# Kernel tuning notes

Hardware: AMD Instinct MI355X
Metric: run time of the kernel (lower is better)

Reference implementation:

```python
import jax, jax.numpy as jnp
import numpy as np

LMAX = 4
NC = (LMAX + 1) ** 2          # 25 spherical coefficients
L0 = LMAX + 1                 # number of m=0 coefficients
SPHERE = 128
CIN1 = 2 * SPHERE             # concat(source, target) channels
HID = 64
HEADS = 8
ALPHA_C = 64
VAL_C = 16
OUT_C = 128
GRID = 2 * (LMAX + 1)         # S2 grid resolution
N_NODES = 2500
N_EDGES = 25000
MAX_ELEM = 90
EDGE_IN = 128 + 2 * 64        # distance basis + src/tgt atom embeddings
M_SIZES = [LMAX - m + 1 for m in range(1, LMAX + 1)]  # l-count per |m|>0
RAD_OUT = L0 * CIN1 + sum(s * CIN1 for s in M_SIZES)  # 3840

def _lm(l, m):
    return l * l + l + m
_p = [_lm(l, 0) for l in range(LMAX + 1)]
for m in range(1, LMAX + 1):
    _p += [_lm(l, -m) for l in range(m, LMAX + 1)]
    _p += [_lm(l, m) for l in range(m, LMAX + 1)]
PERM = np.asarray(_p)             # l-primary -> m-primary
INV_PERM = np.argsort(PERM)       # m-primary -> l-primary
EXPAND = np.concatenate([np.full(2 * l + 1, l) for l in range(LMAX + 1)])

def _layernorm(x, g, b, eps=1e-5):
    mu = jnp.mean(x, axis=-1, keepdims=True)
    var = jnp.mean((x - mu) ** 2, axis=-1, keepdims=True)
    return (x - mu) * jax.lax.rsqrt(var + eps) * g + b

def _so2_conv(xm, fc0_w, fc0_b, wms, cin, mout, extra, rad):
    # xm: [E, NC, cin] in m-primary layout. Per-order SO(2) 'complex' conv.
    E = xm.shape[0]
    x0 = xm[:, :L0].reshape(E, L0 * cin)
    off_rad = L0 * cin
    if rad is not None:
        x0 = x0 * rad[:, :off_rad]
    x0 = x0 @ fc0_w + fc0_b
    x0_extra = None
    if extra:
        x0_extra = x0[:, :extra]
        x0 = x0[:, extra:]
    outs = [x0.reshape(E, L0, mout)]
    off = L0
    for i, sz in enumerate(M_SIZES):
        xb = xm[:, off:off + 2 * sz].reshape(E, 2, sz * cin)
        if rad is not None:
            xb = xb * rad[:, off_rad:off_rad + sz * cin][:, None, :]
            off_rad += sz * cin
        y = xb @ wms[i]                         # [E, 2, 2*mout*sz]
        half = y.shape[-1] // 2
        yr, yi = y[..., :half], y[..., half:]
        o = jnp.stack([yr[:, 0] - yi[:, 1], yr[:, 1] + yi[:, 0]], axis=1)
        outs.append(o.reshape(E, 2 * sz, mout))
        off += 2 * sz
    return jnp.concatenate(outs, axis=1), x0_extra

def _segment_softmax(logits, seg, num_segments):
    mx = jax.ops.segment_max(logits, seg, num_segments=num_segments)
    ex = jnp.exp(logits - mx[seg])
    s = jax.ops.segment_sum(ex, seg, num_segments=num_segments)
    return ex / (s[seg] + 1e-16)

def setup_inputs():
    key = jax.random.key(0)
    ks = iter(jax.random.split(key, 64))
    def nrm(shape, scale=1.0):
        return jax.random.normal(next(ks), shape, dtype=jnp.float32) * scale
    def lin(i, o):
        return nrm((i, o), i ** -0.5)
    inp = {}
    inp['x'] = nrm((N_NODES, NC, SPHERE))
    inp['edge_distance'] = nrm((N_EDGES, 128))
    inp['src_table'] = jax.random.uniform(next(ks), (MAX_ELEM, 64), jnp.float32, -0.001, 0.001)
    inp['tgt_table'] = jax.random.uniform(next(ks), (MAX_ELEM, 64), jnp.float32, -0.001, 0.001)
    inp['rad_w1'] = lin(EDGE_IN, 64); inp['rad_b1'] = jnp.zeros((64,), jnp.float32)
    inp['rad_ln1_g'] = jnp.ones((64,), jnp.float32); inp['rad_ln1_b'] = jnp.zeros((64,), jnp.float32)
    inp['rad_w2'] = lin(64, 64); inp['rad_b2'] = jnp.zeros((64,), jnp.float32)
    inp['rad_ln2_g'] = jnp.ones((64,), jnp.float32); inp['rad_ln2_b'] = jnp.zeros((64,), jnp.float32)
    inp['rad_w3'] = lin(64, RAD_OUT); inp['rad_b3'] = jnp.zeros((RAD_OUT,), jnp.float32)
    inp['wigner'] = nrm((N_EDGES, NC, NC), NC ** -0.5)
    extra1 = HEADS * ALPHA_C + HID
    inp['c1_fc0_w'] = lin(L0 * CIN1, L0 * HID + extra1)
    inp['c1_fc0_b'] = jnp.zeros((L0 * HID + extra1,), jnp.float32)
    for i, sz in enumerate(M_SIZES):
        inp['c1_wm%d' % (i + 1)] = lin(sz * CIN1, 2 * HID * sz)
    inp['to_grid'] = nrm((GRID, GRID, NC), NC ** -0.5)
    inp['from_grid'] = nrm((GRID, GRID, NC), float(GRID * GRID) ** -0.5)
    inp['alpha_ln_g'] = jnp.ones((ALPHA_C,), jnp.float32)
    inp['alpha_ln_b'] = jnp.zeros((ALPHA_C,), jnp.float32)
    std = ALPHA_C ** -0.5
    inp['alpha_dot'] = jax.random.uniform(next(ks), (HEADS, ALPHA_C), jnp.float32, -std, std)
    vout = HEADS * VAL_C
    inp['c2_fc0_w'] = lin(L0 * HID, L0 * vout)
    inp['c2_fc0_b'] = jnp.zeros((L0 * vout,), jnp.float32)
    for i, sz in enumerate(M_SIZES):
        inp['c2_wm%d' % (i + 1)] = lin(sz * HID, 2 * vout * sz)
    inp['proj_w'] = nrm((L0, OUT_C, vout), vout ** -0.5)
    inp['proj_b'] = jnp.zeros((OUT_C,), jnp.float32)
    inp['atomic_numbers'] = jax.random.randint(next(ks), (N_NODES,), 0, MAX_ELEM)
    inp['edge_index'] = jax.random.randint(next(ks), (2, N_EDGES), 0, N_NODES)
    return inp

def reference(x, edge_distance, src_table, tgt_table,
              rad_w1, rad_b1, rad_ln1_g, rad_ln1_b, rad_w2, rad_b2, rad_ln2_g, rad_ln2_b, rad_w3, rad_b3,
              wigner, c1_fc0_w, c1_fc0_b, c1_wm1, c1_wm2, c1_wm3, c1_wm4,
              to_grid, from_grid, alpha_ln_g, alpha_ln_b, alpha_dot,
              c2_fc0_w, c2_fc0_b, c2_wm1, c2_wm2, c2_wm3, c2_wm4, proj_w, proj_b,
              atomic_numbers, edge_index):
    E = edge_index.shape[1]
    N = x.shape[0]
    src, tgt = edge_index[0], edge_index[1]
    # invariant edge scalars: distance basis + source/target atom embeddings
    x_edge = jnp.concatenate([edge_distance, src_table[atomic_numbers[src]], tgt_table[atomic_numbers[tgt]]], axis=1)
    # gather node embeddings to edges, rotate into edge frame (Wigner-D)
    msg = jnp.concatenate([x[src], x[tgt]], axis=2)          # [E, NC, 2*SPHERE]
    msg = jnp.einsum('eml,elc->emc', wigner, msg)
    msg = msg[:, PERM]                                        # m-primary layout
    # radial MLP producing per-(m,l,channel) edge weights
    h = jax.nn.silu(_layernorm(x_edge @ rad_w1 + rad_b1, rad_ln1_g, rad_ln1_b))
    h = jax.nn.silu(_layernorm(h @ rad_w2 + rad_b2, rad_ln2_g, rad_ln2_b))
    rad = h @ rad_w3 + rad_b3                                 # [E, RAD_OUT]
    extra1 = HEADS * ALPHA_C + HID
    msg, x0_extra = _so2_conv(msg, c1_fc0_w, c1_fc0_b, (c1_wm1, c1_wm2, c1_wm3, c1_wm4), CIN1, HID, extra1, rad)
    x0_alpha = x0_extra[:, :HEADS * ALPHA_C]
    x0_gate = x0_extra[:, HEADS * ALPHA_C:]
    # separable S2 activation: scalar SiLU on l=0, grid SiLU on l>0
    msg_l = msg[:, INV_PERM]
    grid = jax.nn.silu(jnp.einsum('bai,eic->ebac', to_grid, msg_l))
    s2 = jnp.einsum('bai,ebac->eic', from_grid, grid)
    msg_l = jnp.concatenate([jax.nn.silu(x0_gate)[:, None, :], s2[:, 1:]], axis=1)
    # second SO(2) conv (internal weights, no radial)
    msg_m = msg_l[:, PERM]
    msg_m, _ = _so2_conv(msg_m, c2_fc0_w, c2_fc0_b, (c2_wm1, c2_wm2, c2_wm3, c2_wm4), HID, HEADS * VAL_C, None, None)
    msg_l = msg_m[:, INV_PERM]
    # attention logits (LayerNorm + SmoothLeakyReLU(0.2) + dot)
    a = _layernorm(x0_alpha.reshape(E, HEADS, ALPHA_C), alpha_ln_g, alpha_ln_b)
    a = 0.6 * a + 0.4 * a * (2.0 * jax.nn.sigmoid(a) - 1.0)
    logits = jnp.einsum('ehk,hk->eh', a, alpha_dot)
    # rotate messages back to global frame (wigner_inv = wigner^T)
    msg_l = jnp.einsum('eml,emc->elc', wigner, msg_l)
    alpha = _segment_softmax(logits, tgt, N)                  # [E, HEADS]
    v = msg_l.reshape(E, NC, HEADS, VAL_C) * alpha[:, None, :, None]
    node = jax.ops.segment_sum(v.reshape(E, NC, HEADS * VAL_C), tgt, num_segments=N)
    # SO3_LinearV2 projection: per-degree linear, bias only on l=0
    out = jnp.einsum('nmi,moi->nmo', node, proj_w[EXPAND])
    out = out.at[:, 0, :].add(proj_b)
    return out
```

## Files before the change

kernel.cpp:

```cpp
#include <hip/hip_runtime.h>
#include <cstddef>

typedef unsigned short u16;
typedef __attribute__((ext_vector_type(8))) short short8;
typedef __attribute__((ext_vector_type(4))) float float4v;

__constant__ int c_PERM[25] = {0,2,6,12,20, 1,5,11,19, 3,7,13,21, 4,10,18, 8,14,22, 9,17, 15,23, 16,24};
__constant__ int c_ROFF[25] = {0,256,512,768,1024, 1280,1536,1792,2048, 1280,1536,1792,2048,
                               2304,2560,2816, 2304,2560,2816, 3072,3328, 3072,3328, 3584,3584};
__constant__ int c_EXPAND[25] = {0,1,1,1,2,2,2,2,2,3,3,3,3,3,3,3,4,4,4,4,4,4,4,4,4};

static constexpr int PERM_CE[25] = {0,2,6,12,20, 1,5,11,19, 3,7,13,21, 4,10,18, 8,14,22, 9,17, 15,23, 16,24};
static constexpr int INV_CE[25]  = {0,5,1,9,13, 6,2,10,16,19, 14,7,3,11,17, 21,23,20,15,8, 4,12,18,22,24};

__device__ __forceinline__ float wsum64(float v){
#pragma unroll
  for(int m=32;m>0;m>>=1) v += __shfl_xor(v, m, 64);
  return v;
}
__device__ __forceinline__ float siluf(float x){ return x/(1.f+expf(-x)); }

__device__ __forceinline__ void bsplit(float v, u16 &h, u16 &l){
  unsigned u = __float_as_uint(v);
  unsigned hb = (u + 0x7FFFu + ((u>>16)&1u)) >> 16;
  h = (u16)hb;
  float r = v - __uint_as_float(hb<<16);
  unsigned u2 = __float_as_uint(r);
  l = (u16)((u2 + 0x7FFFu + ((u2>>16)&1u)) >> 16);
}

__global__ __launch_bounds__(256) void wtrans_kernel(const float* __restrict__ W, u16* __restrict__ Wh, u16* __restrict__ Wl, int K, int C2){
  int idx = blockIdx.x*256 + threadIdx.x;
  int K2 = 2*K;
  if(idx >= C2*K2) return;
  int n = idx / K2, k2 = idx % K2;
  int half = C2>>1;
  float v;
  if(k2 < K) v = W[k2*C2 + n];
  else { int k = k2-K; v = (n<half) ? -W[k*C2 + half + n] : W[k*C2 + n - half]; }
  u16 h,l; bsplit(v,h,l);
  Wh[idx]=h; Wl[idx]=l;
}

__global__ __launch_bounds__(256) void fctrans_kernel(const float* __restrict__ W, u16* __restrict__ Wh, u16* __restrict__ Wl, int K, int N){
  int idx = blockIdx.x*256 + threadIdx.x;
  if(idx >= N*K) return;
  int n = idx / K, k = idx % K;
  u16 h,l; bsplit(W[(size_t)k*N + n],h,l);
  Wh[idx]=h; Wl[idx]=l;
}

__global__ __launch_bounds__(256) void ptrans_kernel(const float* __restrict__ pw, float* __restrict__ pwt){
  int idx = blockIdx.x*256+threadIdx.x;
  if(idx >= 5*16384) return;
  int l = idx>>14, r = idx & 16383, i = r>>7, o = r&127;
  pwt[idx] = pw[(l<<14) + (o<<7) + i];
}

__global__ __launch_bounds__(256) void hist_kernel(const int* __restrict__ tgt_all, int* __restrict__ cnt, int E){
  int idx = blockIdx.x*256+threadIdx.x;
  if(idx>=E) return;
  atomicAdd(&cnt[tgt_all[idx]], 1);
}
__global__ __launch_bounds__(256) void scan_kernel(const int* __restrict__ cnt, int* __restrict__ basearr, int* __restrict__ cur, int NN){
  __shared__ int sh[256];
  __shared__ int carry;
  if(threadIdx.x==0) carry = 0;
  __syncthreads();
  for(int t0=0; t0<NN; t0+=256){
    int i = t0 + threadIdx.x;
    int v = (i<NN)? cnt[i] : 0;
    sh[threadIdx.x]=v; __syncthreads();
    for(int off=1; off<256; off<<=1){
      int add = (threadIdx.x>=off)? sh[threadIdx.x-off]:0; __syncthreads();
      sh[threadIdx.x]+=add; __syncthreads();
    }
    int excl = carry + sh[threadIdx.x]-v;
    if(i<NN){ basearr[i]=excl; cur[i]=excl; }
    __syncthreads();
    if(threadIdx.x==255) carry += sh[255];
    __syncthreads();
  }
}
__global__ __launch_bounds__(256) void scatter_kernel(const int* __restrict__ ei, int* __restrict__ cur,
    int* __restrict__ order, int* __restrict__ srcs, int* __restrict__ tgts, int E){
  int idx = blockIdx.x*256+threadIdx.x;
  if(idx>=E) return;
  int t = ei[E+idx];
  int pos = atomicAdd(&cur[t], 1);
  order[pos] = idx;
  tgts[pos] = t;
  srcs[pos] = ei[idx];
}

__global__ __launch_bounds__(64) void radial_kernel(
    const float* __restrict__ ed, const float* __restrict__ st, const float* __restrict__ tt,
    const float* __restrict__ w1, const float* __restrict__ b1, const float* __restrict__ g1, const float* __restrict__ bb1,
    const float* __restrict__ w2, const float* __restrict__ b2, const float* __restrict__ g2, const float* __restrict__ bb2,
    const int* __restrict__ an, const int* __restrict__ order,
    const int* __restrict__ src, const int* __restrict__ tgt,
    u16* __restrict__ h2h, u16* __restrict__ h2l){
  int e = blockIdx.x; int lane = threadIdx.x;
  __shared__ float xe[256];
  __shared__ float h1s[64];
  int eo = order[e];
  int s = src[e], t = tgt[e];
  xe[lane]      = ed[(size_t)eo*128 + lane];
  xe[64+lane]   = ed[(size_t)eo*128 + 64 + lane];
  int as = an[s], at = an[t];
  xe[128+lane]  = st[as*64 + lane];
  xe[192+lane]  = tt[at*64 + lane];
  __syncthreads();
  float acc = b1[lane];
  for(int k=0;k<256;k++) acc += xe[k]*w1[k*64+lane];
  float mu = wsum64(acc)*(1.f/64.f);
  float d = acc - mu;
  float var = wsum64(d*d)*(1.f/64.f);
  float nrm = d*rsqrtf(var+1e-5f)*g1[lane]+bb1[lane];
  h1s[lane] = siluf(nrm);
  __syncthreads();
  float acc2 = b2[lane];
  for(int k=0;k<64;k++) acc2 += h1s[k]*w2[k*64+lane];
  mu = wsum64(acc2)*(1.f/64.f);
  d = acc2-mu;
  var = wsum64(d*d)*(1.f/64.f);
  nrm = d*rsqrtf(var+1e-5f)*g2[lane]+bb2[lane];
  u16 h,l; bsplit(siluf(nrm),h,l);
  h2h[(size_t)e*64+lane]=h; h2l[(size_t)e*64+lane]=l;
}

struct GrpArgs {
  const u16* Ah[6]; const u16* Al[6];
  const u16* Bh[6]; const u16* Bl[6];
  const float* bias[6]; float* C1[6]; float* C2[6];
  int lda[6]; int K[6]; int ldc1[6]; int ldc2[6]; int split[6];
  int xoff[7]; int ng; int M; int gx; int gy;
};

__global__ __launch_bounds__(256) void mgemm_kernel(GrpArgs a){
  __shared__ __align__(16) u16 Ash[2][4096];
  __shared__ __align__(16) u16 Asl[2][4096];
  __shared__ __align__(16) u16 Bsh[2][4096];
  __shared__ __align__(16) u16 Bsl[2][4096];

  int b = blockIdx.x;
  int xcd = b & 7, i = b >> 3;
  int pbase = a.gx >> 3, prem = a.gx & 7;
  int s = pbase + (xcd < prem ? 1 : 0);
  if(i >= s * a.gy) return;
  int o = xcd*pbase + (xcd < prem ? xcd : prem);
  int xt = o + (i % s);
  int yt = i / s;

  int g = 0;
  while(g+1 < a.ng && xt >= a.xoff[g+1]) g++;
  int n0 = (xt - a.xoff[g])*128, m0 = yt*128;
  const int M = a.M, K = a.K[g], lda = a.lda[g];
  const u16* __restrict__ Ah = a.Ah[g]; const u16* __restrict__ Al = a.Al[g];
  const u16* __restrict__ Bh = a.Bh[g]; const u16* __restrict__ Bl = a.Bl[g];
  int t = threadIdx.x;
  int r0 = t>>2, kblk = t&3, k80 = kblk*8;
  int ar0 = m0 + r0; if(ar0 >= M) ar0 = M-1;
  int ar1 = m0 + r0 + 64; if(ar1 >= M) ar1 = M-1;
  const u16* Ap0h = Ah + (size_t)ar0*lda + k80;
  const u16* Ap1h = Ah + (size_t)ar1*lda + k80;
  const u16* Ap0l = Al + (size_t)ar0*lda + k80;
  const u16* Ap1l = Al + (size_t)ar1*lda + k80;
  const u16* Bp0h = Bh + (size_t)(n0+r0)*K + k80;
  const u16* Bp1h = Bh + (size_t)(n0+r0+64)*K + k80;
  const u16* Bp0l = Bl + (size_t)(n0+r0)*K + k80;
  const u16* Bp1l = Bl + (size_t)(n0+r0+64)*K + k80;
  int pcbS = kblk ^ ((r0>>1)&3);
  int sA = r0*32 + pcbS*8;
  int sB = sA + 64*32;

  int wave = t>>6, lane = t&63;
  int wr = wave>>1, wc = wave&1;
  int ml = lane&15, q = lane>>4;
  int pcbA = q ^ ((ml>>1)&3);
  int aoff = (wr*64 + ml)*32 + pcbA*8;
  int boff = (wc*64 + ml)*32 + pcbA*8;

  float4v acc[4][4];
#pragma unroll
  for(int i2=0;i2<4;i2++)
#pragma unroll
    for(int j=0;j<4;j++) acc[i2][j] = 0.f;

  short8 cva[4], cvb[4];
  cva[0] = *(const short8*)(Ap0h); cva[1] = *(const short8*)(Ap1h);
  cva[2] = *(const short8*)(Ap0l); cva[3] = *(const short8*)(Ap1l);
  cvb[0] = *(const short8*)(Bp0h); cvb[1] = *(const short8*)(Bp1h);
  cvb[2] = *(const short8*)(Bp0l); cvb[3] = *(const short8*)(Bp1l);

  int p = 0;
  for(int k0=0; k0<K; k0+=32){
    *(short8*)(&Ash[p][sA]) = cva[0];
    *(short8*)(&Ash[p][sB]) = cva[1];
    *(short8*)(&Asl[p][sA]) = cva[2];
    *(short8*)(&Asl[p][sB]) = cva[3];
    *(short8*)(&Bsh[p][sA]) = cvb[0];
    *(short8*)(&Bsh[p][sB]) = cvb[1];
    *(short8*)(&Bsl[p][sA]) = cvb[2];
    *(short8*)(&Bsl[p][sB]) = cvb[3];
    __syncthreads();
    if(k0+32 < K){
      int kn = k0+32;
      cva[0] = *(const short8*)(Ap0h + kn); cva[1] = *(const short8*)(Ap1h + kn);
      cva[2] = *(const short8*)(Ap0l + kn); cva[3] = *(const short8*)(Ap1l + kn);
      cvb[0] = *(const short8*)(Bp0h + kn); cvb[1] = *(const short8*)(Bp1h + kn);
      cvb[2] = *(const short8*)(Bp0l + kn); cvb[3] = *(const short8*)(Bp1l + kn);
    }
    short8 afh[4], afl[4];
#pragma unroll
    for(int i2=0;i2<4;i2++){
      afh[i2] = *(const short8*)(&Ash[p][aoff + i2*512]);
      afl[i2] = *(const short8*)(&Asl[p][aoff + i2*512]);
    }
#pragma unroll
    for(int j=0;j<4;j++){
      short8 bfh = *(const short8*)(&Bsh[p][boff + j*512]);
      short8 bfl = *(const short8*)(&Bsl[p][boff + j*512]);
#pragma unroll
      for(int i2=0;i2<4;i2++){
        acc[i2][j] = __builtin_amdgcn_mfma_f32_16x16x32_bf16(afh[i2], bfh, acc[i2][j], 0,0,0);
        acc[i2][j] = __builtin_amdgcn_mfma_f32_16x16x32_bf16(afh[i2], bfl, acc[i2][j], 0,0,0);
        acc[i2][j] = __builtin_amdgcn_mfma_f32_16x16x32_bf16(afl[i2], bfh, acc[i2][j], 0,0,0);
      }
    }
    p ^= 1;
  }
  const float* bias = a.bias[g];
  int split = a.split[g];
  float* C1 = a.C1[g]; float* C2 = a.C2[g];
  int ldc1 = a.ldc1[g], ldc2 = a.ldc2[g];
#pragma unroll
  for(int i2=0;i2<4;i2++){
    int rowb = m0 + wr*64 + i2*16 + q*4;
#pragma unroll
    for(int r=0;r<4;r++){
      int row = rowb + r;
      if(row < M){
#pragma unroll
        for(int j=0;j<4;j++){
          int col = n0 + wc*64 + j*16 + ml;
          float v = acc[i2][j][r];
          if(bias) v += bias[col];
          if(col < split) C1[(size_t)row*ldc1 + col] = v;
          else            C2[(size_t)row*ldc2 + (col-split)] = v;
        }
      }
    }
  }
}

__global__ __launch_bounds__(256) void wigner1_kernel(
    const float* __restrict__ x, const float* __restrict__ wigner_all,
    const int* __restrict__ order, const int* __restrict__ src, const int* __restrict__ tgt,
    const float* __restrict__ rad, u16* __restrict__ msg1h, u16* __restrict__ msg1l){
  int e = blockIdx.x; int t = threadIdx.x;
  __shared__ float wig[625];
  __shared__ float4 cat4[1600];
  int eo = order[e];
  int s = src[e], tg = tgt[e];
  for(int i=t;i<625;i+=256) wig[i] = wigner_all[(size_t)eo*625 + i];
  const float4* xs = (const float4*)(x + (size_t)s*3200);
  const float4* xt = (const float4*)(x + (size_t)tg*3200);
  for(int idx=t; idx<1600; idx+=256){
    int l = idx>>6, slot = idx&63;
    cat4[idx] = (slot<32) ? xs[l*32 + slot] : xt[l*32 + (slot-32)];
  }
  __syncthreads();
  int wave = t>>6, lane = t&63;
  for(int p=wave; p<25; p+=4){
    int pl = c_PERM[p];
    float4 acc = {0.f,0.f,0.f,0.f};
#pragma unroll
    for(int l=0;l<25;l++){
      float w = wig[pl*25 + l];
      float4 c = cat4[l*64 + lane];
      acc.x += w*c.x; acc.y += w*c.y; acc.z += w*c.z; acc.w += w*c.w;
    }
    float4 rd = *(const float4*)(rad + (size_t)e*3840 + c_ROFF[p] + lane*4);
    acc.x*=rd.x; acc.y*=rd.y; acc.z*=rd.z; acc.w*=rd.w;
    u16 h0,h1,h2,h3,l0,l1,l2,l3;
    bsplit(acc.x,h0,l0); bsplit(acc.y,h1,l1); bsplit(acc.z,h2,l2); bsplit(acc.w,h3,l3);
    size_t base = (size_t)e*6400 + p*256 + lane*4;
    *(uint2*)(msg1h + base) = make_uint2((unsigned)h0 | ((unsigned)h1<<16), (unsigned)h2 | ((unsigned)h3<<16));
    *(uint2*)(msg1l + base) = make_uint2((unsigned)l0 | ((unsigned)l1<<16), (unsigned)l2 | ((unsigned)l3<<16));
  }
}

__global__ __launch_bounds__(64) void grid_kernel(
    const float* __restrict__ msg2, const float* __restrict__ x0e,
    const float* __restrict__ tg, const float* __restrict__ fg,
    u16* __restrict__ m2h, u16* __restrict__ m2l){
  int e = blockIdx.x; int lane = threadIdx.x;
  float r[25];
#pragma unroll
  for(int i=0;i<25;i++) r[i] = msg2[((size_t)e*25 + INV_CE[i])*64 + lane];
  float s2[25];
#pragma unroll
  for(int i=0;i<25;i++) s2[i]=0.f;
  for(int g=0; g<100; g++){
    float tv=0.f;
#pragma unroll
    for(int i=0;i<25;i++) tv += tg[g*25+i]*r[i];
    tv = siluf(tv);
#pragma unroll
    for(int i=0;i<25;i++) s2[i] += fg[g*25+i]*tv;
  }
  float gate = siluf(x0e[(size_t)e*576 + 512 + lane]);
#pragma unroll
  for(int p=0;p<25;p++){
    int lp = PERM_CE[p];
    float v = (lp==0) ? gate : s2[lp];
    u16 h,l; bsplit(v,h,l);
    size_t idx = ((size_t)e*25+p)*64 + lane;
    m2h[idx]=h; m2l[idx]=l;
  }
}

__global__ __launch_bounds__(64) void alpha_kernel(
    const float* __restrict__ x0e, const float* __restrict__ g, const float* __restrict__ b,
    const float* __restrict__ adot, const int* __restrict__ tgt,
    float* __restrict__ exb, float* __restrict__ ssum){
  int e = blockIdx.x; int lane = threadIdx.x;
  int t = tgt[e];
  float gg = g[lane], bb = b[lane];
  for(int h=0;h<8;h++){
    float v = x0e[(size_t)e*576 + h*64 + lane];
    float mu = wsum64(v)*(1.f/64.f);
    float d = v-mu;
    float var = wsum64(d*d)*(1.f/64.f);
    float a = d*rsqrtf(var+1e-5f)*gg+bb;
    float sig = 1.f/(1.f+expf(-a));
    float a2 = 0.6f*a + 0.4f*a*(2.f*sig-1.f);
    float p = a2*adot[h*64+lane];
    float lg = wsum64(p);
    if(lane==0){
      float ex = expf(lg);
      exb[e*8+h]=ex;
      atomicAdd(&ssum[t*8+h], ex);
    }
  }
}

__global__ __launch_bounds__(256) void agg_kernel(
    const float* __restrict__ wigner_all, const float* __restrict__ msg3,
    const float* __restrict__ exb, const int* __restrict__ order,
    const int* __restrict__ basearr, const int* __restrict__ cnt,
    float* __restrict__ node, int e0, int e1){
  int n = blockIdx.x; int t = threadIdx.x;
  int b0 = basearr[n], c = cnt[n];
  int lo = b0 > e0 ? b0 : e0;
  int hi = (b0+c) < e1 ? (b0+c) : e1;
  if(lo >= hi) return;
  int lg = t>>5;
  int c4 = t&31;
  __shared__ float wig2[625];
  __shared__ float m3s[3200];
  float4v acc[4];
#pragma unroll
  for(int k=0;k<4;k++) acc[k] = 0.f;
  float* nb = node + (size_t)n*3200;
#pragma unroll
  for(int k=0;k<4;k++){ int l = lg + 8*k; if(l<25) acc[k] = *(const float4v*)(nb + l*128 + c4*4); }
  for(int j=lo;j<hi;j++){
    int e = order[j];
    int el = j - e0;
    __syncthreads();
    for(int i=t;i<625;i+=256){ int q=i/25, l=i%25; wig2[i] = wigner_all[((size_t)e*25 + c_PERM[q])*25 + l]; }
    for(int i=t;i<800;i+=256) ((float4*)m3s)[i] = ((const float4*)(msg3 + (size_t)el*3200))[i];
    __syncthreads();
    float ex = exb[el*8 + (c4>>2)];
    float4v tmp[4];
#pragma unroll
    for(int k=0;k<4;k++) tmp[k] = 0.f;
    for(int q=0;q<25;q++){
      float4v m = *(const float4v*)(m3s + q*128 + c4*4);
#pragma unroll
      for(int k=0;k<4;k++){
        int l = lg + 8*k;
        float w = (l<25) ? wig2[q*25 + l] : 0.f;
        tmp[k] += w*m;
      }
    }
#pragma unroll
    for(int k=0;k<4;k++) acc[k] += ex*tmp[k];
  }
#pragma unroll
  for(int k=0;k<4;k++){ int l = lg + 8*k; if(l<25) *(float4v*)(nb + l*128 + c4*4) = acc[k]; }
}

__global__ __launch_bounds__(256) void proj_kernel(
    const float* __restrict__ node, const float* __restrict__ ssum,
    const float* __restrict__ pwt, const float* __restrict__ proj_b,
    float* __restrict__ out, int NN){
  int n0 = blockIdx.x*2; int t = threadIdx.x;
  __shared__ float nd[2][3200];
  __shared__ float inv[2][8];
  if(t<16){
    int j=t>>3, h=t&7;
    int n=n0+j; if(n>=NN) n=NN-1;
    inv[j][h] = 1.f/(ssum[n*8+h] + 1e-16f);
  }
  __syncthreads();
  int n1 = (n0+1 < NN) ? (n0+1) : (NN-1);
  for(int i=t;i<3200;i+=256){
    int h = (i&127)>>4;
    nd[0][i] = node[(size_t)n0*3200 + i] * inv[0][h];
    nd[1][i] = node[(size_t)n1*3200 + i] * inv[1][h];
  }
  __syncthreads();
  int o = t&127, half = t>>7;
  for(int p=half;p<25;p+=2){
    int l = c_EXPAND[p];
    const float* w = pwt + l*16384;
    float a0=0.f, a1=0.f;
    for(int i=0;i<128;i++){
      float wv = w[i*128+o];
      a0 += nd[0][p*128+i]*wv;
      a1 += nd[1][p*128+i]*wv;
    }
    float bs = (p==0)? proj_b[o] : 0.f;
    out[((size_t)n0*25+p)*128 + o] = a0 + bs;
    if(n0+1 < NN) out[((size_t)(n0+1)*25+p)*128 + o] = a1 + bs;
  }
}

extern "C" void kernel_launch(void* const* d_in, const int* in_sizes, int n_in,
                              void* d_out, int out_size, void* d_ws, size_t ws_size,
                              hipStream_t stream) {
  const float* x           = (const float*)d_in[0];
  const float* edge_dist   = (const float*)d_in[1];
  const float* src_table   = (const float*)d_in[2];
  const float* tgt_table   = (const float*)d_in[3];
  const float* rad_w1      = (const float*)d_in[4];
  const float* rad_b1      = (const float*)d_in[5];
  const float* rad_ln1_g   = (const float*)d_in[6];
  const float* rad_ln1_b   = (const float*)d_in[7];
  const float* rad_w2      = (const float*)d_in[8];
  const float* rad_b2      = (const float*)d_in[9];
  const float* rad_ln2_g   = (const float*)d_in[10];
  const float* rad_ln2_b   = (const float*)d_in[11];
  const float* rad_w3      = (const float*)d_in[12];
  const float* rad_b3      = (const float*)d_in[13];
  const float* wigner      = (const float*)d_in[14];
  const float* c1_fc0_w    = (const float*)d_in[15];
  const float* c1_fc0_b    = (const float*)d_in[16];
  const float* c1_wm[4]    = {(const float*)d_in[17],(const float*)d_in[18],(const float*)d_in[19],(const float*)d_in[20]};
  const float* to_grid     = (const float*)d_in[21];
  const float* from_grid   = (const float*)d_in[22];
  const float* alpha_ln_g  = (const float*)d_in[23];
  const float* alpha_ln_b  = (const float*)d_in[24];
  const float* alpha_dot   = (const float*)d_in[25];
  const float* c2_fc0_w    = (const float*)d_in[26];
  const float* c2_fc0_b    = (const float*)d_in[27];
  const float* c2_wm[4]    = {(const float*)d_in[28],(const float*)d_in[29],(const float*)d_in[30],(const float*)d_in[31]};
  const float* proj_w      = (const float*)d_in[32];
  const float* proj_b      = (const float*)d_in[33];
  const int*   atomic_nums = (const int*)d_in[34];
  const int*   edge_index  = (const int*)d_in[35];
  float* out = (float*)d_out;
  (void)n_in; (void)out_size;

  const int E  = in_sizes[35]/2;
  const int NN = in_sizes[34];

  const int K1[4] = {1024, 768, 512, 256}, C1c[4] = {512, 384, 256, 128};
  const int K2[4] = {256, 192, 128, 64},  C2c[4] = {1024, 768, 512, 256};
  const size_t W3T = 3840*64;
  const size_t FC1 = 896*1280;
  const size_t W1S[4] = {512*2048, 384*1536, 256*1024, 128*512};
  const size_t FC2 = 640*320;
  const size_t W2S[4] = {1024*512, 768*384, 512*256, 256*128};
  const size_t WSUM = W3T + FC1 + W1S[0]+W1S[1]+W1S[2]+W1S[3] + FC2 + W2S[0]+W2S[1]+W2S[2]+W2S[3];
  const size_t persist = (size_t)NN*8 + (size_t)NN*3200 + WSUM
                       + 81920 + (size_t)3*NN + (size_t)3*E + 8192;
  const size_t wfl = ws_size / sizeof(float);
  const int copts[10] = {25000, 12500, 6250, 5000, 3125, 2500, 1250, 625, 250, 125};
  int C = 125;
  for(int i=0;i<10;i++){
    size_t hc = (size_t)(copts[i]+1)/2;
    size_t need = (size_t)copts[i]*(6400+576+8) + hc*3840 + persist;
    if(need <= wfl){ C = copts[i]; break; }
  }
  const int nch = (E + C - 1)/C;
  const size_t halfC = (size_t)(C+1)/2;

  float* ws = (float*)d_ws;
  u16* msg1h = (u16*)ws;
  u16* msg1l = msg1h + (size_t)C*6400;
  u16* m2h   = (u16*)ws;
  u16* m2l   = m2h + (size_t)C*1600;
  float* msg3 = ws + (size_t)C*1600;
  float* rad  = ws + (size_t)C*6400;
  float* msg2 = rad;
  float* x0e  = rad + halfC*3840;
  u16* h2h = (u16*)x0e;
  u16* h2l = h2h + halfC*64;
  float* exb  = x0e + (size_t)C*576;
  float* ssum = exb + (size_t)C*8;
  float* node = ssum + (size_t)NN*8;
  u16* wb = (u16*)(node + (size_t)NN*3200);
  u16 *w3h = wb, *w3l = w3h + W3T;
  u16 *f1h = w3l + W3T, *f1l = f1h + FC1;
  u16 *w1h[4], *w1l[4];
  u16* p = f1l + FC1;
  for(int i=0;i<4;i++){ w1h[i]=p; w1l[i]=p+W1S[i]; p += 2*W1S[i]; }
  u16 *f2h = p, *f2l = f2h + FC2; p = f2l + FC2;
  u16 *w2h[4], *w2l[4];
  for(int i=0;i<4;i++){ w2h[i]=p; w2l[i]=p+W2S[i]; p += 2*W2S[i]; }
  float* pwt = (float*)p;
  int* cntb  = (int*)(pwt + 81920);
  int* baseb = cntb + NN;
  int* curb  = baseb + NN;
  int* order = curb + NN;
  int* srcs  = order + E;
  int* tgts  = srcs + E;

  hipMemsetAsync(node, 0, (size_t)NN*3200*sizeof(float), stream);
  hipMemsetAsync(ssum, 0, (size_t)NN*8*sizeof(float), stream);
  hipMemsetAsync(cntb, 0, (size_t)NN*sizeof(int), stream);

  hist_kernel<<<(E+255)/256, 256, 0, stream>>>(edge_index + E, cntb, E);
  scan_kernel<<<1, 256, 0, stream>>>(cntb, baseb, curb, NN);
  scatter_kernel<<<(E+255)/256, 256, 0, stream>>>(edge_index, curb, order, srcs, tgts, E);

  fctrans_kernel<<<((int)W3T+255)/256, 256, 0, stream>>>(rad_w3, w3h, w3l, 64, 3840);
  fctrans_kernel<<<((int)FC1+255)/256, 256, 0, stream>>>(c1_fc0_w, f1h, f1l, 1280, 896);
  fctrans_kernel<<<((int)FC2+255)/256, 256, 0, stream>>>(c2_fc0_w, f2h, f2l, 320, 640);
  for(int i=0;i<4;i++)
    wtrans_kernel<<<((int)W1S[i]*2+255)/256, 256, 0, stream>>>(c1_wm[i], w1h[i], w1l[i], K1[i], C1c[i]);
  for(int i=0;i<4;i++)
    wtrans_kernel<<<((int)W2S[i]*2+255)/256, 256, 0, stream>>>(c2_wm[i], w2h[i], w2l[i], K2[i], C2c[i]);
  ptrans_kernel<<<320, 256, 0, stream>>>(proj_w, pwt);

  auto launchM = [&](GrpArgs &ga, int gx, int gy){
    ga.gx = gx; ga.gy = gy;
    int base = gx>>3, rem = gx&7;
    int maxs = base + (rem?1:0);
    mgemm_kernel<<<8*maxs*gy, 256, 0, stream>>>(ga);
  };

  const int OFF1[4] = {5,13,19,23};
  for(int ch=0; ch<nch; ch++){
    int e0 = ch*C;
    int ce = (E - e0 < C) ? (E - e0) : C;
    int mt = (ce+127)/128;

    int half1 = (ce+1)/2;
    for(int hh=0; hh<2; hh++){
      int h0 = hh ? half1 : 0;
      int he = hh ? (ce - half1) : half1;
      if(he <= 0) continue;
      radial_kernel<<<he, 64, 0, stream>>>(edge_dist, src_table, tgt_table,
          rad_w1, rad_b1, rad_ln1_g, rad_ln1_b, rad_w2, rad_b2, rad_ln2_g, rad_ln2_b,
          atomic_nums, order + e0 + h0, srcs + e0 + h0, tgts + e0 + h0, h2h, h2l);
      {
        GrpArgs ga = {};
        ga.ng = 1; ga.M = he;
        ga.Ah[0]=h2h; ga.Al[0]=h2l; ga.Bh[0]=w3h; ga.Bl[0]=w3l;
        ga.bias[0]=rad_b3; ga.C1[0]=rad; ga.C2[0]=nullptr;
        ga.lda[0]=64; ga.K[0]=64; ga.ldc1[0]=3840; ga.ldc2[0]=0; ga.split[0]=3840;
        ga.xoff[0]=0; ga.xoff[1]=30;
        launchM(ga, 30, (he+127)/128);
      }
      wigner1_kernel<<<he, 256, 0, stream>>>(x, wigner, order + e0 + h0, srcs + e0 + h0, tgts + e0 + h0,
          rad, msg1h + (size_t)h0*6400, msg1l + (size_t)h0*6400);
    }

    {
      GrpArgs ga = {};
      ga.ng = 5; ga.M = ce;
      ga.Ah[0]=msg1h; ga.Al[0]=msg1l; ga.Bh[0]=f1h; ga.Bl[0]=f1l;
      ga.bias[0]=c1_fc0_b; ga.C1[0]=x0e; ga.C2[0]=msg2;
      ga.lda[0]=6400; ga.K[0]=1280; ga.ldc1[0]=576; ga.ldc2[0]=1600; ga.split[0]=576;
      int xo = 7;
      ga.xoff[0]=0; ga.xoff[1]=7;
      for(int i=0;i<4;i++){
        int gidx = i+1;
        ga.Ah[gidx]=msg1h + (size_t)OFF1[i]*256; ga.Al[gidx]=msg1l + (size_t)OFF1[i]*256;
        ga.Bh[gidx]=w1h[i]; ga.Bl[gidx]=w1l[i];
        ga.bias[gidx]=nullptr; ga.C1[gidx]=msg2 + OFF1[i]*64; ga.C2[gidx]=nullptr;
        ga.lda[gidx]=6400; ga.K[gidx]=2*K1[i]; ga.ldc1[gidx]=1600; ga.ldc2[gidx]=0; ga.split[gidx]=C1c[i];
        xo += C1c[i]/128;
        ga.xoff[gidx+1]=xo;
      }
      launchM(ga, xo, mt);
    }

    grid_kernel<<<ce, 64, 0, stream>>>(msg2, x0e, to_grid, from_grid, m2h, m2l);
    alpha_kernel<<<ce, 64, 0, stream>>>(x0e, alpha_ln_g, alpha_ln_b, alpha_dot, tgts + e0, exb, ssum);

    {
      GrpArgs ga = {};
      ga.ng = 5; ga.M = ce;
      ga.Ah[0]=m2h; ga.Al[0]=m2l; ga.Bh[0]=f2h; ga.Bl[0]=f2l;
      ga.bias[0]=c2_fc0_b; ga.C1[0]=msg3; ga.C2[0]=nullptr;
      ga.lda[0]=1600; ga.K[0]=320; ga.ldc1[0]=3200; ga.ldc2[0]=0; ga.split[0]=640;
      int xo = 5;
      ga.xoff[0]=0; ga.xoff[1]=5;
      for(int i=0;i<4;i++){
        int gidx = i+1;
        ga.Ah[gidx]=m2h + (size_t)OFF1[i]*64; ga.Al[gidx]=m2l + (size_t)OFF1[i]*64;
        ga.Bh[gidx]=w2h[i]; ga.Bl[gidx]=w2l[i];
        ga.bias[gidx]=nullptr; ga.C1[gidx]=msg3 + OFF1[i]*128; ga.C2[gidx]=nullptr;
        ga.lda[gidx]=1600; ga.K[gidx]=2*K2[i]; ga.ldc1[gidx]=3200; ga.ldc2[gidx]=0; ga.split[gidx]=C2c[i];
        xo += C2c[i]/128;
        ga.xoff[gidx+1]=xo;
      }
      launchM(ga, xo, mt);
    }

    agg_kernel<<<NN, 256, 0, stream>>>(wigner, msg3, exb, order, baseb, cntb, node, e0, e0+ce);
  }

  proj_kernel<<<(NN+1)/2, 256, 0, stream>>>(node, ssum, pwt, proj_b, out, NN);
}
```

Baseline: 3.540 ms.

## Store msg1 low residual as 8-bit float to shrink workspace and enlarge chunks

The low-order bf16 residual of the first SO(2) conv input is now encoded as a custom 8-bit float (sign, 5-bit exponent, 2-bit mantissa) instead of a second bf16 array, and decoded back to bf16 inside the GEMM A-tile load. This cuts msg1 storage and the read traffic for the largest GEMM. The freed workspace lets the chunk size be computed directly from available memory, with the radial stage split into four sub-chunks, so fewer chunks and launches are needed. The cost is some extra decode ALU work in the GEMM loader and slightly lower accuracy in the split-bf16 emulation.

```diff
diff --git a/kernel.cpp b/kernel.cpp
--- a/kernel.cpp
+++ b/kernel.cpp
@@ -2,7 +2,9 @@
 #include <cstddef>
 
 typedef unsigned short u16;
+typedef unsigned char u8;
 typedef __attribute__((ext_vector_type(8))) short short8;
+typedef __attribute__((ext_vector_type(8))) unsigned char uchar8;
 typedef __attribute__((ext_vector_type(4))) float float4v;
 
 __constant__ int c_PERM[25] = {0,2,6,12,20, 1,5,11,19, 3,7,13,21, 4,10,18, 8,14,22, 9,17, 15,23, 16,24};
@@ -27,6 +29,30 @@
   float r = v - __uint_as_float(hb<<16);
   unsigned u2 = __float_as_uint(r);
   l = (u16)((u2 + 0x7FFFu + ((u2>>16)&1u)) >> 16);
+}
+
+__device__ __forceinline__ u8 enc_q(float r){
+  unsigned b = __float_as_uint(r);
+  unsigned s = (b>>24)&0x80u;
+  int e = (b>>23)&0xFF;
+  unsigned m = b&0x7FFFFFu;
+  int ef = e - 104;
+  if(ef <= 0) return (u8)s;
+  unsigned m2 = (m + 0xFFFFFu + ((m>>21)&1u)) >> 21;
+  if(m2 >= 4){ m2 = 0; ef++; }
+  if(ef >= 31){ ef = 30; m2 = 3; }
+  return (u8)(s | ((unsigned)ef<<2) | m2);
+}
+__device__ __forceinline__ short8 dec8(uchar8 q){
+  short8 r;
+#pragma unroll
+  for(int i=0;i<8;i++){
+    unsigned b = (unsigned)q[i];
+    unsigned ef = (b>>2)&31u;
+    unsigned v = ((b&0x80u)<<8) | (((b&0x7Fu)<<5) + (104u<<7));
+    r[i] = (short)(ef ? v : ((b&0x80u)<<8));
+  }
+  return r;
 }
 
 __global__ __launch_bounds__(256) void wtrans_kernel(const float* __restrict__ W, u16* __restrict__ Wh, u16* __restrict__ Wl, int K, int C2){
@@ -131,6 +157,7 @@
 
 struct GrpArgs {
   const u16* Ah[6]; const u16* Al[6];
+  const u8*  Aq[6];
   const u16* Bh[6]; const u16* Bl[6];
   const float* bias[6]; float* C1[6]; float* C2[6];
   int lda[6]; int K[6]; int ldc1[6]; int ldc2[6]; int split[6];
@@ -156,7 +183,10 @@
   while(g+1 < a.ng && xt >= a.xoff[g+1]) g++;
   int n0 = (xt - a.xoff[g])*128, m0 = yt*128;
   const int M = a.M, K = a.K[g], lda = a.lda[g];
-  const u16* __restrict__ Ah = a.Ah[g]; const u16* __restrict__ Al = a.Al[g];
+  const u16* __restrict__ Ah = a.Ah[g];
+  const u8*  __restrict__ Aq = a.Aq[g];
+  const bool qa = (Aq != nullptr);
+  const u16* __restrict__ Al = qa ? a.Ah[g] : a.Al[g];
   const u16* __restrict__ Bh = a.Bh[g]; const u16* __restrict__ Bl = a.Bl[g];
   int t = threadIdx.x;
   int r0 = t>>2, kblk = t&3, k80 = kblk*8;
@@ -166,6 +196,8 @@
   const u16* Ap1h = Ah + (size_t)ar1*lda + k80;
   const u16* Ap0l = Al + (size_t)ar0*lda + k80;
   const u16* Ap1l = Al + (size_t)ar1*lda + k80;
+  const u8*  Aq0  = qa ? (Aq + (size_t)ar0*lda + k80) : nullptr;
+  const u8*  Aq1  = qa ? (Aq + (size_t)ar1*lda + k80) : nullptr;
   const u16* Bp0h = Bh + (size_t)(n0+r0)*K + k80;
   const u16* Bp1h = Bh + (size_t)(n0+r0+64)*K + k80;
   const u16* Bp0l = Bl + (size_t)(n0+r0)*K + k80;
@@ -189,7 +221,8 @@
 
   short8 cva[4], cvb[4];
   cva[0] = *(const short8*)(Ap0h); cva[1] = *(const short8*)(Ap1h);
-  cva[2] = *(const short8*)(Ap0l); cva[3] = *(const short8*)(Ap1l);
+  if(qa){ cva[2] = dec8(*(const uchar8*)(Aq0)); cva[3] = dec8(*(const uchar8*)(Aq1)); }
+  else  { cva[2] = *(const short8*)(Ap0l);      cva[3] = *(const short8*)(Ap1l); }
   cvb[0] = *(const short8*)(Bp0h); cvb[1] = *(const short8*)(Bp1h);
   cvb[2] = *(const short8*)(Bp0l); cvb[3] = *(const short8*)(Bp1l);
 
@@ -207,7 +240,8 @@
     if(k0+32 < K){
       int kn = k0+32;
       cva[0] = *(const short8*)(Ap0h + kn); cva[1] = *(const short8*)(Ap1h + kn);
-      cva[2] = *(const short8*)(Ap0l + kn); cva[3] = *(const short8*)(Ap1l + kn);
+      if(qa){ cva[2] = dec8(*(const uchar8*)(Aq0 + kn)); cva[3] = dec8(*(const uchar8*)(Aq1 + kn)); }
+      else  { cva[2] = *(const short8*)(Ap0l + kn);      cva[3] = *(const short8*)(Ap1l + kn); }
       cvb[0] = *(const short8*)(Bp0h + kn); cvb[1] = *(const short8*)(Bp1h + kn);
       cvb[2] = *(const short8*)(Bp0l + kn); cvb[3] = *(const short8*)(Bp1l + kn);
     }
@@ -257,7 +291,7 @@
 __global__ __launch_bounds__(256) void wigner1_kernel(
     const float* __restrict__ x, const float* __restrict__ wigner_all,
     const int* __restrict__ order, const int* __restrict__ src, const int* __restrict__ tgt,
-    const float* __restrict__ rad, u16* __restrict__ msg1h, u16* __restrict__ msg1l){
+    const float* __restrict__ rad, u16* __restrict__ msg1h, u8* __restrict__ msg1q){
   int e = blockIdx.x; int t = threadIdx.x;
   __shared__ float wig[625];
   __shared__ float4 cat4[1600];
@@ -283,11 +317,19 @@
     }
     float4 rd = *(const float4*)(rad + (size_t)e*3840 + c_ROFF[p] + lane*4);
     acc.x*=rd.x; acc.y*=rd.y; acc.z*=rd.z; acc.w*=rd.w;
-    u16 h0,h1,h2,h3,l0,l1,l2,l3;
-    bsplit(acc.x,h0,l0); bsplit(acc.y,h1,l1); bsplit(acc.z,h2,l2); bsplit(acc.w,h3,l3);
+    float vv[4] = {acc.x, acc.y, acc.z, acc.w};
+    u16 hh[4]; u8 qq[4];
+#pragma unroll
+    for(int c=0;c<4;c++){
+      unsigned u = __float_as_uint(vv[c]);
+      unsigned hb = (u + 0x7FFFu + ((u>>16)&1u)) >> 16;
+      hh[c] = (u16)hb;
+      float r = vv[c] - __uint_as_float(hb<<16);
+      qq[c] = enc_q(r);
+    }
     size_t base = (size_t)e*6400 + p*256 + lane*4;
-    *(uint2*)(msg1h + base) = make_uint2((unsigned)h0 | ((unsigned)h1<<16), (unsigned)h2 | ((unsigned)h3<<16));
-    *(uint2*)(msg1l + base) = make_uint2((unsigned)l0 | ((unsigned)l1<<16), (unsigned)l2 | ((unsigned)l3<<16));
+    *(uint2*)(msg1h + base) = make_uint2((unsigned)hh[0] | ((unsigned)hh[1]<<16), (unsigned)hh[2] | ((unsigned)hh[3]<<16));
+    *(unsigned*)(msg1q + base) = (unsigned)qq[0] | ((unsigned)qq[1]<<8) | ((unsigned)qq[2]<<16) | ((unsigned)qq[3]<<24);
   }
 }
 
@@ -477,29 +519,36 @@
   const size_t W2S[4] = {1024*512, 768*384, 512*256, 256*128};
   const size_t WSUM = W3T + FC1 + W1S[0]+W1S[1]+W1S[2]+W1S[3] + FC2 + W2S[0]+W2S[1]+W2S[2]+W2S[3];
   const size_t persist = (size_t)NN*8 + (size_t)NN*3200 + WSUM
-                       + 81920 + (size_t)3*NN + (size_t)3*E + 8192;
+                       + 81920 + (size_t)3*NN + (size_t)3*E + 16384;
   const size_t wfl = ws_size / sizeof(float);
-  const int copts[10] = {25000, 12500, 6250, 5000, 3125, 2500, 1250, 625, 250, 125};
-  int C = 125;
-  for(int i=0;i<10;i++){
-    size_t hc = (size_t)(copts[i]+1)/2;
-    size_t need = (size_t)copts[i]*(6400+576+8) + hc*3840 + persist;
-    if(need <= wfl){ C = copts[i]; break; }
+
+  int C = 512;
+  if(wfl > persist){
+    size_t avail = wfl - persist;
+    long long c0 = (long long)(avail / 7944);
+    if(c0 > E) c0 = E;
+    while(c0 > 512){
+      size_t qc = ((size_t)c0+3)/4;
+      size_t need = (size_t)c0*4800 + qc*3840 + (size_t)c0*1600 + (size_t)c0*576 + (size_t)c0*8;
+      if(need <= avail) break;
+      c0 -= 64;
+    }
+    C = (int)c0;
   }
   const int nch = (E + C - 1)/C;
-  const size_t halfC = (size_t)(C+1)/2;
+  const size_t qcap = ((size_t)C+3)/4;
 
   float* ws = (float*)d_ws;
   u16* msg1h = (u16*)ws;
-  u16* msg1l = msg1h + (size_t)C*6400;
+  u8*  msg1q = (u8*)(ws + (size_t)C*3200);
   u16* m2h   = (u16*)ws;
   u16* m2l   = m2h + (size_t)C*1600;
   float* msg3 = ws + (size_t)C*1600;
-  float* rad  = ws + (size_t)C*6400;
-  float* msg2 = rad;
-  float* x0e  = rad + halfC*3840;
+  float* rad  = ws + (size_t)C*4800;
+  float* msg2 = rad + qcap*3840;
+  float* x0e  = msg2 + (size_t)C*1600;
   u16* h2h = (u16*)x0e;
-  u16* h2l = h2h + halfC*64;
+  u16* h2l = h2h + qcap*64;
   float* exb  = x0e + (size_t)C*576;
   float* ssum = exb + (size_t)C*8;
   float* node = ssum + (size_t)NN*8;
@@ -550,38 +599,39 @@
     int ce = (E - e0 < C) ? (E - e0) : C;
     int mt = (ce+127)/128;
 
-    int half1 = (ce+1)/2;
-    for(int hh=0; hh<2; hh++){
-      int h0 = hh ? half1 : 0;
-      int he = hh ? (ce - half1) : half1;
-      if(he <= 0) continue;
+    for(int sc=0; sc<4; sc++){
+      int h0 = sc*(int)qcap;
+      if(h0 >= ce) break;
+      int he = (ce - h0 < (int)qcap) ? (ce - h0) : (int)qcap;
       radial_kernel<<<he, 64, 0, stream>>>(edge_dist, src_table, tgt_table,
           rad_w1, rad_b1, rad_ln1_g, rad_ln1_b, rad_w2, rad_b2, rad_ln2_g, rad_ln2_b,
           atomic_nums, order + e0 + h0, srcs + e0 + h0, tgts + e0 + h0, h2h, h2l);
       {
         GrpArgs ga = {};
         ga.ng = 1; ga.M = he;
-        ga.Ah[0]=h2h; ga.Al[0]=h2l; ga.Bh[0]=w3h; ga.Bl[0]=w3l;
+        ga.Ah[0]=h2h; ga.Al[0]=h2l; ga.Aq[0]=nullptr; ga.Bh[0]=w3h; ga.Bl[0]=w3l;
         ga.bias[0]=rad_b3; ga.C1[0]=rad; ga.C2[0]=nullptr;
         ga.lda[0]=64; ga.K[0]=64; ga.ldc1[0]=3840; ga.ldc2[0]=0; ga.split[0]=3840;
         ga.xoff[0]=0; ga.xoff[1]=30;
         launchM(ga, 30, (he+127)/128);
       }
       wigner1_kernel<<<he, 256, 0, stream>>>(x, wigner, order + e0 + h0, srcs + e0 + h0, tgts + e0 + h0,
-          rad, msg1h + (size_t)h0*6400, msg1l + (size_t)h0*6400);
+          rad, msg1h + (size_t)h0*6400, msg1q + (size_t)h0*6400);
     }
 
     {
       GrpArgs ga = {};
       ga.ng = 5; ga.M = ce;
-      ga.Ah[0]=msg1h; ga.Al[0]=msg1l; ga.Bh[0]=f1h; ga.Bl[0]=f1l;
+      ga.Ah[0]=msg1h; ga.Al[0]=nullptr; ga.Aq[0]=msg1q; ga.Bh[0]=f1h; ga.Bl[0]=f1l;
       ga.bias[0]=c1_fc0_b; ga.C1[0]=x0e; ga.C2[0]=msg2;
       ga.lda[0]=6400; ga.K[0]=1280; ga.ldc1[0]=576; ga.ldc2[0]=1600; ga.split[0]=576;
       int xo = 7;
       ga.xoff[0]=0; ga.xoff[1]=7;
       for(int i=0;i<4;i++){
         int gidx = i+1;
-        ga.Ah[gidx]=msg1h + (size_t)OFF1[i]*256; ga.Al[gidx]=msg1l + (size_t)OFF1[i]*256;
+        ga.Ah[gidx]=msg1h + (size_t)OFF1[i]*256;
+        ga.Al[gidx]=nullptr;
+        ga.Aq[gidx]=msg1q + (size_t)OFF1[i]*256;
         ga.Bh[gidx]=w1h[i]; ga.Bl[gidx]=w1l[i];
         ga.bias[gidx]=nullptr; ga.C1[gidx]=msg2 + OFF1[i]*64; ga.C2[gidx]=nullptr;
         ga.lda[gidx]=6400; ga.K[gidx]=2*K1[i]; ga.ldc1[gidx]=1600; ga.ldc2[gidx]=0; ga.split[gidx]=C1c[i];
@@ -597,14 +647,14 @@
     {
       GrpArgs ga = {};
       ga.ng = 5; ga.M = ce;
-      ga.Ah[0]=m2h; ga.Al[0]=m2l; ga.Bh[0]=f2h; ga.Bl[0]=f2l;
+      ga.Ah[0]=m2h; ga.Al[0]=m2l; ga.Aq[0]=nullptr; ga.Bh[0]=f2h; ga.Bl[0]=f2l;
       ga.bias[0]=c2_fc0_b; ga.C1[0]=msg3; ga.C2[0]=nullptr;
       ga.lda[0]=1600; ga.K[0]=320; ga.ldc1[0]=3200; ga.ldc2[0]=0; ga.split[0]=640;
       int xo = 5;
       ga.xoff[0]=0; ga.xoff[1]=5;
       for(int i=0;i<4;i++){
         int gidx = i+1;
-        ga.Ah[gidx]=m2h + (size_t)OFF1[i]*64; ga.Al[gidx]=m2l + (size_t)OFF1[i]*64;
+        ga.Ah[gidx]=m2h + (size_t)OFF1[i]*64; ga.Al[gidx]=m2l + (size_t)OFF1[i]*64; ga.Aq[gidx]=nullptr;
         ga.Bh[gidx]=w2h[i]; ga.Bl[gidx]=w2l[i];
         ga.bias[gidx]=nullptr; ga.C1[gidx]=msg3 + OFF1[i]*128; ga.C2[gidx]=nullptr;
         ga.lda[gidx]=1600; ga.K[gidx]=2*K2[i]; ga.ldc1[gidx]=3200; ga.ldc2[gidx]=0; ga.split[gidx]=C2c[i];
```

Result: slower. 3.833 ms (+8.3%).

## Split-K the first SO(2) grouped GEMM, swizzle tiles by row across XCDs, resize chunks

Applied to the files above, without the earlier changes.

The per-order complex GEMMs in the first SO(2) conv are split along K into 512-wide slices. The first slice writes directly into msg2 and the others write partial sums into a new buffer, which a new reduce_kernel adds back into msg2. This balances work across tile groups whose K ranges from 512 to 2048. The block-to-XCD mapping now distributes M tiles rather than N tiles across the 8 XCDs, the second GEMM's groups are reordered, and the chunk size C is derived from workspace capacity instead of a fixed list. The cost is extra partial-sum traffic and one more launch per chunk.

```diff
diff --git a/kernel.cpp b/kernel.cpp
--- a/kernel.cpp
+++ b/kernel.cpp
@@ -129,12 +129,13 @@
   h2h[(size_t)e*64+lane]=h; h2l[(size_t)e*64+lane]=l;
 }
 
+#define MAXG 11
 struct GrpArgs {
-  const u16* Ah[6]; const u16* Al[6];
-  const u16* Bh[6]; const u16* Bl[6];
-  const float* bias[6]; float* C1[6]; float* C2[6];
-  int lda[6]; int K[6]; int ldc1[6]; int ldc2[6]; int split[6];
-  int xoff[7]; int ng; int M; int gx; int gy;
+  const u16* Ah[MAXG]; const u16* Al[MAXG];
+  const u16* Bh[MAXG]; const u16* Bl[MAXG];
+  const float* bias[MAXG]; float* C1[MAXG]; float* C2[MAXG];
+  int lda[MAXG]; int K[MAXG]; int ldb[MAXG]; int ldc1[MAXG]; int ldc2[MAXG]; int split[MAXG];
+  int xoff[MAXG+1]; int ng; int M; int gx; int gy;
 };
 
 __global__ __launch_bounds__(256) void mgemm_kernel(GrpArgs a){
@@ -145,17 +146,17 @@
 
   int b = blockIdx.x;
   int xcd = b & 7, i = b >> 3;
-  int pbase = a.gx >> 3, prem = a.gx & 7;
-  int s = pbase + (xcd < prem ? 1 : 0);
-  if(i >= s * a.gy) return;
-  int o = xcd*pbase + (xcd < prem ? xcd : prem);
-  int xt = o + (i % s);
-  int yt = i / s;
+  int ybase = a.gy >> 3, yrem = a.gy & 7;
+  int sy = ybase + (xcd < yrem ? 1 : 0);
+  if(i >= sy * a.gx) return;
+  int oy = xcd*ybase + (xcd < yrem ? xcd : yrem);
+  int yt = oy + i / a.gx;
+  int xt = i % a.gx;
 
   int g = 0;
   while(g+1 < a.ng && xt >= a.xoff[g+1]) g++;
   int n0 = (xt - a.xoff[g])*128, m0 = yt*128;
-  const int M = a.M, K = a.K[g], lda = a.lda[g];
+  const int M = a.M, K = a.K[g], lda = a.lda[g], ldb = a.ldb[g];
   const u16* __restrict__ Ah = a.Ah[g]; const u16* __restrict__ Al = a.Al[g];
   const u16* __restrict__ Bh = a.Bh[g]; const u16* __restrict__ Bl = a.Bl[g];
   int t = threadIdx.x;
@@ -166,10 +167,10 @@
   const u16* Ap1h = Ah + (size_t)ar1*lda + k80;
   const u16* Ap0l = Al + (size_t)ar0*lda + k80;
   const u16* Ap1l = Al + (size_t)ar1*lda + k80;
-  const u16* Bp0h = Bh + (size_t)(n0+r0)*K + k80;
-  const u16* Bp1h = Bh + (size_t)(n0+r0+64)*K + k80;
-  const u16* Bp0l = Bl + (size_t)(n0+r0)*K + k80;
-  const u16* Bp1l = Bl + (size_t)(n0+r0+64)*K + k80;
+  const u16* Bp0h = Bh + (size_t)(n0+r0)*ldb + k80;
+  const u16* Bp1h = Bh + (size_t)(n0+r0+64)*ldb + k80;
+  const u16* Bp0l = Bl + (size_t)(n0+r0)*ldb + k80;
+  const u16* Bp1l = Bl + (size_t)(n0+r0+64)*ldb + k80;
   int pcbS = kblk ^ ((r0>>1)&3);
   int sA = r0*32 + pcbS*8;
   int sB = sA + 64*32;
@@ -251,6 +252,28 @@
         }
       }
     }
+  }
+}
+
+__global__ __launch_bounds__(256) void reduce_kernel(
+    float* __restrict__ msg2, const float* __restrict__ P, int ce, int Ccap){
+  int idx = blockIdx.x*256+threadIdx.x;
+  if(idx >= ce*1152) return;
+  int row = idx/1152, c = idx%1152;
+  const float* P1 = P;
+  const float* P2 = P + (size_t)3*Ccap*512;
+  const float* P3 = P2 + (size_t)2*Ccap*384;
+  if(c < 512){
+    float s = P1[(size_t)row*512 + c] + P1[(size_t)Ccap*512 + (size_t)row*512 + c]
+            + P1[(size_t)2*Ccap*512 + (size_t)row*512 + c];
+    msg2[(size_t)row*1600 + 320 + c] += s;
+  } else if(c < 896){
+    int c2 = c-512;
+    float s = P2[(size_t)row*384 + c2] + P2[(size_t)Ccap*384 + (size_t)row*384 + c2];
+    msg2[(size_t)row*1600 + 832 + c2] += s;
+  } else {
+    int c3 = c-896;
+    msg2[(size_t)row*1600 + 1216 + c3] += P3[(size_t)row*256 + c3];
   }
 }
 
@@ -477,14 +500,16 @@
   const size_t W2S[4] = {1024*512, 768*384, 512*256, 256*128};
   const size_t WSUM = W3T + FC1 + W1S[0]+W1S[1]+W1S[2]+W1S[3] + FC2 + W2S[0]+W2S[1]+W2S[2]+W2S[3];
   const size_t persist = (size_t)NN*8 + (size_t)NN*3200 + WSUM
-                       + 81920 + (size_t)3*NN + (size_t)3*E + 8192;
+                       + 81920 + (size_t)3*NN + (size_t)3*E + 16384;
   const size_t wfl = ws_size / sizeof(float);
-  const int copts[10] = {25000, 12500, 6250, 5000, 3125, 2500, 1250, 625, 250, 125};
-  int C = 125;
-  for(int i=0;i<10;i++){
-    size_t hc = (size_t)(copts[i]+1)/2;
-    size_t need = (size_t)copts[i]*(6400+576+8) + hc*3840 + persist;
-    if(need <= wfl){ C = copts[i]; break; }
+
+  int C = 512;
+  if(wfl > persist + 512*11464){
+    long long c0 = (long long)((wfl - persist) / 11464);
+    if(c0 > E) c0 = E;
+    c0 &= ~255LL;
+    if(c0 < 512) c0 = 512;
+    C = (int)c0;
   }
   const int nch = (E + C - 1)/C;
   const size_t halfC = (size_t)(C+1)/2;
@@ -501,7 +526,8 @@
   u16* h2h = (u16*)x0e;
   u16* h2l = h2h + halfC*64;
   float* exb  = x0e + (size_t)C*576;
-  float* ssum = exb + (size_t)C*8;
+  float* pbuf = exb + (size_t)C*8;
+  float* ssum = pbuf + (size_t)C*2560;
   float* node = ssum + (size_t)NN*8;
   u16* wb = (u16*)(node + (size_t)NN*3200);
   u16 *w3h = wb, *w3l = w3h + W3T;
@@ -539,12 +565,15 @@
 
   auto launchM = [&](GrpArgs &ga, int gx, int gy){
     ga.gx = gx; ga.gy = gy;
-    int base = gx>>3, rem = gx&7;
-    int maxs = base + (rem?1:0);
-    mgemm_kernel<<<8*maxs*gy, 256, 0, stream>>>(ga);
+    int ybase = gy>>3, yrem = gy&7;
+    int maxsy = ybase + (yrem?1:0);
+    mgemm_kernel<<<8*maxsy*gx, 256, 0, stream>>>(ga);
   };
 
   const int OFF1[4] = {5,13,19,23};
+  const int KSP1[4] = {4,3,2,1};
+  float* PP[4] = {pbuf, pbuf + (size_t)3*C*512, pbuf + (size_t)3*C*512 + (size_t)2*C*384, nullptr};
+
   for(int ch=0; ch<nch; ch++){
     int e0 = ch*C;
     int ce = (E - e0 < C) ? (E - e0) : C;
@@ -563,7 +592,7 @@
         ga.ng = 1; ga.M = he;
         ga.Ah[0]=h2h; ga.Al[0]=h2l; ga.Bh[0]=w3h; ga.Bl[0]=w3l;
         ga.bias[0]=rad_b3; ga.C1[0]=rad; ga.C2[0]=nullptr;
-        ga.lda[0]=64; ga.K[0]=64; ga.ldc1[0]=3840; ga.ldc2[0]=0; ga.split[0]=3840;
+        ga.lda[0]=64; ga.K[0]=64; ga.ldb[0]=64; ga.ldc1[0]=3840; ga.ldc2[0]=0; ga.split[0]=3840;
         ga.xoff[0]=0; ga.xoff[1]=30;
         launchM(ga, 30, (he+127)/128);
       }
@@ -573,44 +602,56 @@
 
     {
       GrpArgs ga = {};
-      ga.ng = 5; ga.M = ce;
-      ga.Ah[0]=msg1h; ga.Al[0]=msg1l; ga.Bh[0]=f1h; ga.Bl[0]=f1l;
-      ga.bias[0]=c1_fc0_b; ga.C1[0]=x0e; ga.C2[0]=msg2;
-      ga.lda[0]=6400; ga.K[0]=1280; ga.ldc1[0]=576; ga.ldc2[0]=1600; ga.split[0]=576;
-      int xo = 7;
-      ga.xoff[0]=0; ga.xoff[1]=7;
+      ga.M = ce;
+      int g = 0, xo = 0;
+      ga.Ah[g]=msg1h; ga.Al[g]=msg1l; ga.Bh[g]=f1h; ga.Bl[g]=f1l;
+      ga.bias[g]=c1_fc0_b; ga.C1[g]=x0e; ga.C2[g]=msg2;
+      ga.lda[g]=6400; ga.K[g]=1280; ga.ldb[g]=1280; ga.ldc1[g]=576; ga.ldc2[g]=1600; ga.split[g]=576;
+      ga.xoff[g]=xo; xo += 7; g++;
       for(int i=0;i<4;i++){
-        int gidx = i+1;
-        ga.Ah[gidx]=msg1h + (size_t)OFF1[i]*256; ga.Al[gidx]=msg1l + (size_t)OFF1[i]*256;
-        ga.Bh[gidx]=w1h[i]; ga.Bl[gidx]=w1l[i];
-        ga.bias[gidx]=nullptr; ga.C1[gidx]=msg2 + OFF1[i]*64; ga.C2[gidx]=nullptr;
-        ga.lda[gidx]=6400; ga.K[gidx]=2*K1[i]; ga.ldc1[gidx]=1600; ga.ldc2[gidx]=0; ga.split[gidx]=C1c[i];
-        xo += C1c[i]/128;
-        ga.xoff[gidx+1]=xo;
+        int N = C1c[i], Kfull = 2*K1[i];
+        for(int s=0; s<KSP1[i]; s++){
+          ga.Ah[g]=msg1h + (size_t)OFF1[i]*256 + (size_t)s*512;
+          ga.Al[g]=msg1l + (size_t)OFF1[i]*256 + (size_t)s*512;
+          ga.Bh[g]=w1h[i] + (size_t)s*512; ga.Bl[g]=w1l[i] + (size_t)s*512;
+          ga.bias[g]=nullptr; ga.C2[g]=nullptr;
+          ga.lda[g]=6400; ga.K[g]=512; ga.ldb[g]=Kfull; ga.ldc2[g]=0; ga.split[g]=N;
+          if(s==0){ ga.C1[g]=msg2 + OFF1[i]*64; ga.ldc1[g]=1600; }
+          else    { ga.C1[g]=PP[i] + (size_t)(s-1)*C*N; ga.ldc1[g]=N; }
+          ga.xoff[g]=xo; xo += N/128; g++;
+        }
       }
+      ga.ng = g; ga.xoff[g] = xo;
       launchM(ga, xo, mt);
     }
+    reduce_kernel<<<(ce*1152+255)/256, 256, 0, stream>>>(msg2, pbuf, ce, C);
 
     grid_kernel<<<ce, 64, 0, stream>>>(msg2, x0e, to_grid, from_grid, m2h, m2l);
     alpha_kernel<<<ce, 64, 0, stream>>>(x0e, alpha_ln_g, alpha_ln_b, alpha_dot, tgts + e0, exb, ssum);
 
     {
       GrpArgs ga = {};
-      ga.ng = 5; ga.M = ce;
-      ga.Ah[0]=m2h; ga.Al[0]=m2l; ga.Bh[0]=f2h; ga.Bl[0]=f2l;
-      ga.bias[0]=c2_fc0_b; ga.C1[0]=msg3; ga.C2[0]=nullptr;
-      ga.lda[0]=1600; ga.K[0]=320; ga.ldc1[0]=3200; ga.ldc2[0]=0; ga.split[0]=640;
-      int xo = 5;
-      ga.xoff[0]=0; ga.xoff[1]=5;
-      for(int i=0;i<4;i++){
-        int gidx = i+1;
-        ga.Ah[gidx]=m2h + (size_t)OFF1[i]*64; ga.Al[gidx]=m2l + (size_t)OFF1[i]*64;
-        ga.Bh[gidx]=w2h[i]; ga.Bl[gidx]=w2l[i];
-        ga.bias[gidx]=nullptr; ga.C1[gidx]=msg3 + OFF1[i]*128; ga.C2[gidx]=nullptr;
-        ga.lda[gidx]=1600; ga.K[gidx]=2*K2[i]; ga.ldc1[gidx]=3200; ga.ldc2[gidx]=0; ga.split[gidx]=C2c[i];
-        xo += C2c[i]/128;
-        ga.xoff[gidx+1]=xo;
+      ga.M = ce;
+      int ord[5] = {1,2,0,3,4};
+      int g = 0, xo = 0;
+      for(int oi=0; oi<5; oi++){
+        int sel = ord[oi];
+        if(sel == 0){
+          ga.Ah[g]=m2h; ga.Al[g]=m2l; ga.Bh[g]=f2h; ga.Bl[g]=f2l;
+          ga.bias[g]=c2_fc0_b; ga.C1[g]=msg3; ga.C2[g]=nullptr;
+          ga.lda[g]=1600; ga.K[g]=320; ga.ldb[g]=320; ga.ldc1[g]=3200; ga.ldc2[g]=0; ga.split[g]=640;
+          ga.xoff[g]=xo; xo += 5; g++;
+        } else {
+          int i = sel-1;
+          int N = C2c[i], Kfull = 2*K2[i];
+          ga.Ah[g]=m2h + (size_t)OFF1[i]*64; ga.Al[g]=m2l + (size_t)OFF1[i]*64;
+          ga.Bh[g]=w2h[i]; ga.Bl[g]=w2l[i];
+          ga.bias[g]=nullptr; ga.C1[g]=msg3 + OFF1[i]*128; ga.C2[g]=nullptr;
+          ga.lda[g]=1600; ga.K[g]=Kfull; ga.ldb[g]=Kfull; ga.ldc1[g]=3200; ga.ldc2[g]=0; ga.split[g]=N;
+          ga.xoff[g]=xo; xo += N/128; g++;
+        }
       }
+      ga.ng = g; ga.xoff[g] = xo;
       launchM(ga, xo, mt);
     }
 
```

Result: slower. 3.982 ms (+12.5%).
